# Optimization experiments

Hardware: AMD Instinct MI355X
Metric: run time of the kernel (lower is better)

## Reference

```python
import jax, jax.numpy as jnp
import numpy as np


def setup_inputs() -> dict:
    key = jax.random.key(0)
    k1, k2, k3, k4 = jax.random.split(key, 4)
    B, T, F_in, F_out, N, E, K = 16, 64, 64, 64, 128, 2, 4
    x = jax.random.normal(k1, (B, T, F_in, N), dtype=jnp.float32)
    # graph shift operator per (batch, time, edge-feature); scaled to keep powers bounded
    S = jax.random.normal(k2, (B, T, E, N, N), dtype=jnp.float32) / np.sqrt(N)
    H = jax.random.normal(k3, (F_out, E, K, F_in), dtype=jnp.float32) * 0.02
    bias = jax.random.normal(k4, (F_out, 1), dtype=jnp.float32) * 0.02
    return {"x": x, "S": S, "H": H, "bias": bias}


def reference(x, S, H, bias):
    # x: [B,T,F_in,N], S: [B,T,E,N,N], H: [F_out,E,K,F_in], bias: [F_out,1]
    B, T, F_in, N = x.shape
    E = S.shape[2]
    F_out, _, K, _ = H.shape
    # replicate features across edge-feature dim: [B,T,E,F_in,N]
    cur = jnp.broadcast_to(x[:, :, None], (B, T, E, F_in, N))
    taps = [cur]
    zero_row = jnp.zeros((B, 1, E, F_in, N), dtype=x.dtype)
    for _ in range(1, K):
        # time-shift: tap k at time t depends on tap k-1 at time t-1
        cur = jnp.concatenate([zero_row, cur[:, :-1]], axis=1)
        # diffuse over graph: [..,F_in,N] @ [..,N,N]
        cur = jnp.matmul(cur, S)
        taps.append(cur)
    z = jnp.stack(taps, axis=2)  # [B,T,K,E,F_in,N]
    # [B,T,N, E*K*F_in], matching permute(0,1,5,3,2,4) in the source
    z = z.transpose(0, 1, 5, 3, 2, 4).reshape(B, T, N, E * K * F_in)
    Hm = H.reshape(F_out, E * K * F_in)
    y = jnp.einsum('btnf,of->bton', z, Hm)  # [B,T,F_out,N]
    return y + bias  # bias [F_out,1] broadcasts over N
```

## Files before the change

kernel.cpp:

```cpp
#include <hip/hip_runtime.h>


namespace {
constexpr int B = 16, T = 64, F = 64, N = 128, E = 2, K = 4;
constexpr int SSW = 136;
constexpr int SXW = 68;
constexpr int SZW = 136;
constexpr int TC = 8;
}

typedef short v8s __attribute__((ext_vector_type(8)));
typedef float v4f __attribute__((ext_vector_type(4)));

__device__ inline ushort f2bf(float f) {
  union { float f; uint u; } v; v.f = f;
  uint u = v.u;
  return (ushort)((u + 0x7fffu + ((u >> 16) & 1u)) >> 16);
}

__device__ inline uint pk2(float a, float b) {
  return (uint)f2bf(a) | ((uint)f2bf(b) << 16);
}

__global__ __launch_bounds__(256, 2) void gf_fused(
    const float* __restrict__ x, const float* __restrict__ S,
    const float* __restrict__ H, const float* __restrict__ bias,
    float* __restrict__ y) {
  __shared__ ushort sS[128 * SSW];
  __shared__ ushort sX[128 * SXW];
  __shared__ ushort sSt[6][16 * SZW];
  const int g = blockIdx.x;
  const int xcd = g & 7, loc = g >> 3;
  const int os = loc & 3, unitL = loc >> 2;
  const int unit = xcd * 16 + unitL;
  const int b = unit >> 3, chunk = unit & 7;
  const int t0 = chunk * TC;
  const int ob = os * 16;
  const int tid = threadIdx.x, w = tid >> 6, lane = tid & 63;
  const int l15 = lane & 15, q = lane >> 4;

  for (int i = tid; i < 6 * 16 * SZW; i += 256) ((ushort*)sSt)[i] = 0;

  v4f Yac[2];
  Yac[0][0] = 0.f; Yac[0][1] = 0.f; Yac[0][2] = 0.f; Yac[0][3] = 0.f;
  Yac[1] = Yac[0];

  const int tstart = (t0 == 0) ? 0 : t0 - 3;
  for (int t = tstart; t < t0 + TC; ++t) {
    const bool skipS = (t0 != 0) && (t == t0 - 3);
    const bool emit = (t >= t0);

    {
      const float* xg = x + (size_t)(b * T + t) * (F * N);
      float4 r0[4], r1[4];
      #pragma unroll
      for (int it = 0; it < 4; ++it) {
        const int idx = tid + it * 256;
        const int m = idx >> 4, g2 = idx & 15;
        r0[it] = *(const float4*)(xg + m * N + g2 * 8);
        r1[it] = *(const float4*)(xg + m * N + g2 * 8 + 4);
      }
      #pragma unroll
      for (int it = 0; it < 4; ++it) {
        const int idx = tid + it * 256;
        const int m = idx >> 4, g2 = idx & 15;
        uint4 wv;
        wv.x = pk2(r0[it].x, r0[it].y); wv.y = pk2(r0[it].z, r0[it].w);
        wv.z = pk2(r1[it].x, r1[it].y); wv.w = pk2(r1[it].z, r1[it].w);
        *(uint4*)&sS[m * SSW + ((g2 ^ (m >> 3)) * 8)] = wv;
      }
      __syncthreads();
      const int bb = tid & 7, a2 = (tid >> 3) & 15, hh = tid >> 7;
      v8s rows[8];
      #pragma unroll
      for (int j = 0; j < 8; ++j)
        rows[j] = *(const v8s*)&sS[(8 * bb + j) * SSW + ((a2 ^ bb) * 8)];
      #pragma unroll
      for (int i = 0; i < 4; ++i) {
        const int e2 = 4 * hh + i;
        const int n = 8 * a2 + e2;
        uint4 wv;
        wv.x = (uint)(ushort)rows[0][e2] | ((uint)(ushort)rows[1][e2] << 16);
        wv.y = (uint)(ushort)rows[2][e2] | ((uint)(ushort)rows[3][e2] << 16);
        wv.z = (uint)(ushort)rows[4][e2] | ((uint)(ushort)rows[5][e2] << 16);
        wv.w = (uint)(ushort)rows[6][e2] | ((uint)(ushort)rows[7][e2] << 16);
        *(uint4*)&sX[n * SXW + 8 * bb] = wv;
      }
      __syncthreads();
    }

    for (int e = 0; e < E; ++e) {
      if (!skipS) {
        const float* Sg = S + (size_t)((b * T + t) * E + e) * (N * N);
        #pragma unroll
        for (int half = 0; half < 2; ++half) {
          float4 r0[4], r1[4];
          #pragma unroll
          for (int it = 0; it < 4; ++it) {
            const int idx = tid + (half * 4 + it) * 256;
            const int m = idx >> 4, g2 = idx & 15;
            r0[it] = *(const float4*)(Sg + m * N + g2 * 8);
            r1[it] = *(const float4*)(Sg + m * N + g2 * 8 + 4);
          }
          #pragma unroll
          for (int it = 0; it < 4; ++it) {
            const int idx = tid + (half * 4 + it) * 256;
            const int m = idx >> 4, g2 = idx & 15;
            uint4 wv;
            wv.x = pk2(r0[it].x, r0[it].y); wv.y = pk2(r0[it].z, r0[it].w);
            wv.z = pk2(r1[it].x, r1[it].y); wv.w = pk2(r1[it].z, r1[it].w);
            *(uint4*)&sS[m * SSW + ((g2 ^ (m >> 3)) * 8)] = wv;
          }
        }
      }

      v4f Pn[2], Qn[2], U3n[2];
      #pragma unroll
      for (int mt = 0; mt < 2; ++mt) {
        Pn[mt][0] = 0.f; Pn[mt][1] = 0.f; Pn[mt][2] = 0.f; Pn[mt][3] = 0.f;
        Qn[mt] = Pn[mt]; U3n[mt] = Pn[mt];
      }
      {
        const float* hrow = H + ((size_t)(ob + l15) * E + e) * K * F;
        v8s xf[2][2];
        #pragma unroll
        for (int mt = 0; mt < 2; ++mt)
          #pragma unroll
          for (int fk = 0; fk < 2; ++fk)
            xf[mt][fk] = *(const v8s*)&sX[((2 * w + mt) * 16 + l15) * SXW +
                                          fk * 32 + q * 8];
        #pragma unroll
        for (int k = 0; k < 4; ++k) {
          if (k == 0 && !emit) continue;
          v8s hf[2];
          #pragma unroll
          for (int fk = 0; fk < 2; ++fk) {
            const int f0 = fk * 32 + q * 8;
            const float4 h0 = *(const float4*)(hrow + k * F + f0);
            const float4 h1 = *(const float4*)(hrow + k * F + f0 + 4);
            uint4 u;
            u.x = pk2(h0.x, h0.y); u.y = pk2(h0.z, h0.w);
            u.z = pk2(h1.x, h1.y); u.w = pk2(h1.z, h1.w);
            union { uint4 u; v8s s; } cv; cv.u = u;
            hf[fk] = cv.s;
          }
          v4f* tgt = (k == 0) ? Yac : (k == 1 ? Pn : (k == 2 ? Qn : U3n));
          #pragma unroll
          for (int fk = 0; fk < 2; ++fk)
            #pragma unroll
            for (int mt = 0; mt < 2; ++mt)
              tgt[mt] = __builtin_amdgcn_mfma_f32_16x16x32_bf16(
                  xf[mt][fk], hf[fk], tgt[mt], 0, 0, 0);
        }
      }

      if (!skipS) {
        __syncthreads();
        const int a2 = tid & 15, bg = tid >> 4;
        v8s rows[8];
        #pragma unroll
        for (int j = 0; j < 8; ++j)
          rows[j] = *(const v8s*)&sS[(8 * a2 + j) * SSW + ((bg ^ a2) * 8)];
        __syncthreads();
        #pragma unroll
        for (int i = 0; i < 8; ++i) {
          uint4 wv;
          wv.x = (uint)(ushort)rows[0][i] | ((uint)(ushort)rows[1][i] << 16);
          wv.y = (uint)(ushort)rows[2][i] | ((uint)(ushort)rows[3][i] << 16);
          wv.z = (uint)(ushort)rows[4][i] | ((uint)(ushort)rows[5][i] << 16);
          wv.w = (uint)(ushort)rows[6][i] | ((uint)(ushort)rows[7][i] << 16);
          *(uint4*)&sS[(8 * bg + i) * SSW + ((a2 ^ bg) * 8)] = wv;
        }
        __syncthreads();
        #pragma unroll
        for (int c = 0; c < 4; ++c) {
          const int p = ((4 * c + q) + 2 * l15) & 15;
          const int sbase = l15 * SZW + p * 8;
          const v8s bzP = *(const v8s*)&sSt[e * 3 + 0][sbase];
          const v8s bzQ = *(const v8s*)&sSt[e * 3 + 1][sbase];
          const v8s bzU = *(const v8s*)&sSt[e * 3 + 2][sbase];
          #pragma unroll
          for (int mt = 0; mt < 2; ++mt) {
            const int n = (2 * w + mt) * 16 + l15;
            const v8s af = *(const v8s*)&sS[n * SSW +
                                            ((((c << 2) | q) ^ (n >> 3)) * 8)];
            if (emit)
              Yac[mt] = __builtin_amdgcn_mfma_f32_16x16x32_bf16(
                  af, bzP, Yac[mt], 0, 0, 0);
            Pn[mt] = __builtin_amdgcn_mfma_f32_16x16x32_bf16(
                af, bzQ, Pn[mt], 0, 0, 0);
            Qn[mt] = __builtin_amdgcn_mfma_f32_16x16x32_bf16(
                af, bzU, Qn[mt], 0, 0, 0);
          }
        }
      }

      __syncthreads();
      #pragma unroll
      for (int mt = 0; mt < 2; ++mt) {
        const int cc = (2 * w + mt) * 2 + (q >> 1), h = q & 1;
        const int p = (cc + 2 * l15) & 15;
        const int base = l15 * SZW + p * 8 + h * 4;
        uint2 wv;
        wv.x = pk2(Pn[mt][0], Pn[mt][1]); wv.y = pk2(Pn[mt][2], Pn[mt][3]);
        *(uint2*)&sSt[e * 3 + 0][base] = wv;
        wv.x = pk2(Qn[mt][0], Qn[mt][1]); wv.y = pk2(Qn[mt][2], Qn[mt][3]);
        *(uint2*)&sSt[e * 3 + 1][base] = wv;
        wv.x = pk2(U3n[mt][0], U3n[mt][1]); wv.y = pk2(U3n[mt][2], U3n[mt][3]);
        *(uint2*)&sSt[e * 3 + 2][base] = wv;
      }

      if (e == 1 && emit) {
        float* yg = y + (size_t)(b * T + t) * (F * N);
        const float bv = bias[ob + l15];
        #pragma unroll
        for (int mt = 0; mt < 2; ++mt) {
          float4 v;
          v.x = Yac[mt][0] + bv; v.y = Yac[mt][1] + bv;
          v.z = Yac[mt][2] + bv; v.w = Yac[mt][3] + bv;
          *(float4*)(yg + (ob + l15) * N + (2 * w + mt) * 16 + q * 4) = v;
          Yac[mt][0] = 0.f; Yac[mt][1] = 0.f;
          Yac[mt][2] = 0.f; Yac[mt][3] = 0.f;
        }
      }
    }
  }
}

extern "C" void kernel_launch(void* const* d_in, const int* in_sizes, int n_in,
                              void* d_out, int out_size, void* d_ws, size_t ws_size,
                              hipStream_t stream) {
  const float* x    = (const float*)d_in[0];
  const float* S    = (const float*)d_in[1];
  const float* H    = (const float*)d_in[2];
  const float* bias = (const float*)d_in[3];
  float* y = (float*)d_out;
  (void)d_ws; (void)ws_size;

  gf_fused<<<512, 256, 0, stream>>>(x, S, H, bias, y);
}
```

Before: 335.1 us.

## Pre-transpose x and H to bf16 in prep kernel and prefetch S into registers

```diff
diff --git a/kernel.cpp b/kernel.cpp
--- a/kernel.cpp
+++ b/kernel.cpp
@@ -4,7 +4,6 @@
 namespace {
 constexpr int B = 16, T = 64, F = 64, N = 128, E = 2, K = 4;
 constexpr int SSW = 136;
-constexpr int SXW = 68;
 constexpr int SZW = 136;
 constexpr int TC = 8;
 }
@@ -22,12 +21,70 @@
   return (uint)f2bf(a) | ((uint)f2bf(b) << 16);
 }
 
+__device__ inline void tr64x128(const float* __restrict__ src,
+                                ushort* __restrict__ dst, int dstride,
+                                ushort* sh, int tid) {
+  float4 r0[4], r1[4];
+  #pragma unroll
+  for (int it = 0; it < 4; ++it) {
+    const int idx = tid + it * 256;
+    const int m = idx >> 4, g = idx & 15;
+    r0[it] = *(const float4*)(src + m * N + g * 8);
+    r1[it] = *(const float4*)(src + m * N + g * 8 + 4);
+  }
+  #pragma unroll
+  for (int it = 0; it < 4; ++it) {
+    const int idx = tid + it * 256;
+    const int m = idx >> 4, g = idx & 15;
+    uint4 wv;
+    wv.x = pk2(r0[it].x, r0[it].y); wv.y = pk2(r0[it].z, r0[it].w);
+    wv.z = pk2(r1[it].x, r1[it].y); wv.w = pk2(r1[it].z, r1[it].w);
+    *(uint4*)&sh[m * SSW + ((g ^ (m >> 3)) * 8)] = wv;
+  }
+  __syncthreads();
+  const int bb = tid & 7, a = (tid >> 3) & 15, hh = tid >> 7;
+  v8s rows[8];
+  #pragma unroll
+  for (int j = 0; j < 8; ++j)
+    rows[j] = *(const v8s*)&sh[(8 * bb + j) * SSW + ((a ^ bb) * 8)];
+  #pragma unroll
+  for (int i = 0; i < 4; ++i) {
+    const int e = 4 * hh + i;
+    const int n = 8 * a + e;
+    uint4 wv;
+    wv.x = (uint)(ushort)rows[0][e] | ((uint)(ushort)rows[1][e] << 16);
+    wv.y = (uint)(ushort)rows[2][e] | ((uint)(ushort)rows[3][e] << 16);
+    wv.z = (uint)(ushort)rows[4][e] | ((uint)(ushort)rows[5][e] << 16);
+    wv.w = (uint)(ushort)rows[6][e] | ((uint)(ushort)rows[7][e] << 16);
+    *(uint4*)(dst + n * dstride + 8 * bb) = wv;
+  }
+}
+
+__global__ __launch_bounds__(256) void gf_prep(
+    const float* __restrict__ x, const float* __restrict__ H,
+    ushort* __restrict__ xT, ushort* __restrict__ Hb) {
+  __shared__ ushort sh[64 * SSW];
+  const int bid = blockIdx.x;
+  const int tid = threadIdx.x;
+  if (bid < B * T) {
+    tr64x128(x + (size_t)bid * F * N, xT + (size_t)bid * N * F, F, sh, tid);
+  } else {
+    const int hb = bid - B * T;
+    const int d = (hb * 256 + tid) * 4;
+    const int f = d & 63, o = (d >> 6) & 63, k = (d >> 12) & 3, e = (d >> 14) & 1;
+    const float4 v = *(const float4*)(H + (((size_t)o * E + e) * K + k) * F + f);
+    uint2 wv;
+    wv.x = pk2(v.x, v.y);
+    wv.y = pk2(v.z, v.w);
+    *(uint2*)(Hb + d) = wv;
+  }
+}
+
 __global__ __launch_bounds__(256, 2) void gf_fused(
-    const float* __restrict__ x, const float* __restrict__ S,
-    const float* __restrict__ H, const float* __restrict__ bias,
+    const float* __restrict__ S, const ushort* __restrict__ xT,
+    const ushort* __restrict__ Hb, const float* __restrict__ bias,
     float* __restrict__ y) {
   __shared__ ushort sS[128 * SSW];
-  __shared__ ushort sX[128 * SXW];
   __shared__ ushort sSt[6][16 * SZW];
   const int g = blockIdx.x;
   const int xcd = g & 7, loc = g >> 3;
@@ -46,70 +103,45 @@
   Yac[1] = Yac[0];
 
   const int tstart = (t0 == 0) ? 0 : t0 - 3;
+  const int tS0 = (t0 == 0) ? 0 : t0 - 2;
+
+  float4 pf0[8], pf1[8];
+  {
+    const float* Sg = S + (size_t)((b * T + tS0) * E + 0) * (N * N);
+    #pragma unroll
+    for (int j = 0; j < 8; ++j) {
+      const int idx = tid + j * 256;
+      const int m = idx >> 4, g2 = idx & 15;
+      pf0[j] = *(const float4*)(Sg + m * N + g2 * 8);
+      pf1[j] = *(const float4*)(Sg + m * N + g2 * 8 + 4);
+    }
+  }
+  __syncthreads();
+
   for (int t = tstart; t < t0 + TC; ++t) {
-    const bool skipS = (t0 != 0) && (t == t0 - 3);
+    const bool staged = (t >= tS0);
     const bool emit = (t >= t0);
-
-    {
-      const float* xg = x + (size_t)(b * T + t) * (F * N);
-      float4 r0[4], r1[4];
-      #pragma unroll
-      for (int it = 0; it < 4; ++it) {
-        const int idx = tid + it * 256;
-        const int m = idx >> 4, g2 = idx & 15;
-        r0[it] = *(const float4*)(xg + m * N + g2 * 8);
-        r1[it] = *(const float4*)(xg + m * N + g2 * 8 + 4);
-      }
-      #pragma unroll
-      for (int it = 0; it < 4; ++it) {
-        const int idx = tid + it * 256;
-        const int m = idx >> 4, g2 = idx & 15;
-        uint4 wv;
-        wv.x = pk2(r0[it].x, r0[it].y); wv.y = pk2(r0[it].z, r0[it].w);
-        wv.z = pk2(r1[it].x, r1[it].y); wv.w = pk2(r1[it].z, r1[it].w);
-        *(uint4*)&sS[m * SSW + ((g2 ^ (m >> 3)) * 8)] = wv;
-      }
-      __syncthreads();
-      const int bb = tid & 7, a2 = (tid >> 3) & 15, hh = tid >> 7;
-      v8s rows[8];
-      #pragma unroll
-      for (int j = 0; j < 8; ++j)
-        rows[j] = *(const v8s*)&sS[(8 * bb + j) * SSW + ((a2 ^ bb) * 8)];
-      #pragma unroll
-      for (int i = 0; i < 4; ++i) {
-        const int e2 = 4 * hh + i;
-        const int n = 8 * a2 + e2;
-        uint4 wv;
-        wv.x = (uint)(ushort)rows[0][e2] | ((uint)(ushort)rows[1][e2] << 16);
-        wv.y = (uint)(ushort)rows[2][e2] | ((uint)(ushort)rows[3][e2] << 16);
-        wv.z = (uint)(ushort)rows[4][e2] | ((uint)(ushort)rows[5][e2] << 16);
-        wv.w = (uint)(ushort)rows[6][e2] | ((uint)(ushort)rows[7][e2] << 16);
-        *(uint4*)&sX[n * SXW + 8 * bb] = wv;
-      }
-      __syncthreads();
-    }
-
     for (int e = 0; e < E; ++e) {
-      if (!skipS) {
-        const float* Sg = S + (size_t)((b * T + t) * E + e) * (N * N);
-        #pragma unroll
-        for (int half = 0; half < 2; ++half) {
-          float4 r0[4], r1[4];
-          #pragma unroll
-          for (int it = 0; it < 4; ++it) {
-            const int idx = tid + (half * 4 + it) * 256;
+      if (staged) {
+        #pragma unroll
+        for (int j = 0; j < 8; ++j) {
+          const int idx = tid + j * 256;
+          const int m = idx >> 4, g2 = idx & 15;
+          uint4 wv;
+          wv.x = pk2(pf0[j].x, pf0[j].y); wv.y = pk2(pf0[j].z, pf0[j].w);
+          wv.z = pk2(pf1[j].x, pf1[j].y); wv.w = pk2(pf1[j].z, pf1[j].w);
+          *(uint4*)&sS[m * SSW + ((g2 ^ (m >> 3)) * 8)] = wv;
+        }
+        const int nt = (e == 0) ? t : t + 1;
+        const int ne = (e == 0) ? 1 : 0;
+        if (nt < t0 + TC) {
+          const float* Sg = S + (size_t)((b * T + nt) * E + ne) * (N * N);
+          #pragma unroll
+          for (int j = 0; j < 8; ++j) {
+            const int idx = tid + j * 256;
             const int m = idx >> 4, g2 = idx & 15;
-            r0[it] = *(const float4*)(Sg + m * N + g2 * 8);
-            r1[it] = *(const float4*)(Sg + m * N + g2 * 8 + 4);
-          }
-          #pragma unroll
-          for (int it = 0; it < 4; ++it) {
-            const int idx = tid + (half * 4 + it) * 256;
-            const int m = idx >> 4, g2 = idx & 15;
-            uint4 wv;
-            wv.x = pk2(r0[it].x, r0[it].y); wv.y = pk2(r0[it].z, r0[it].w);
-            wv.z = pk2(r1[it].x, r1[it].y); wv.w = pk2(r1[it].z, r1[it].w);
-            *(uint4*)&sS[m * SSW + ((g2 ^ (m >> 3)) * 8)] = wv;
+            pf0[j] = *(const float4*)(Sg + m * N + g2 * 8);
+            pf1[j] = *(const float4*)(Sg + m * N + g2 * 8 + 4);
           }
         }
       }
@@ -121,29 +153,21 @@
         Qn[mt] = Pn[mt]; U3n[mt] = Pn[mt];
       }
       {
-        const float* hrow = H + ((size_t)(ob + l15) * E + e) * K * F;
+        const ushort* xrow = xT + (size_t)(b * T + t) * (N * F);
         v8s xf[2][2];
         #pragma unroll
         for (int mt = 0; mt < 2; ++mt)
           #pragma unroll
           for (int fk = 0; fk < 2; ++fk)
-            xf[mt][fk] = *(const v8s*)&sX[((2 * w + mt) * 16 + l15) * SXW +
-                                          fk * 32 + q * 8];
+            xf[mt][fk] = *(const v8s*)(xrow + ((2 * w + mt) * 16 + l15) * F +
+                                       fk * 32 + q * 8);
         #pragma unroll
         for (int k = 0; k < 4; ++k) {
           if (k == 0 && !emit) continue;
+          const ushort* hrow = Hb + ((size_t)((e * K + k) * 64) + ob + l15) * 64;
           v8s hf[2];
-          #pragma unroll
-          for (int fk = 0; fk < 2; ++fk) {
-            const int f0 = fk * 32 + q * 8;
-            const float4 h0 = *(const float4*)(hrow + k * F + f0);
-            const float4 h1 = *(const float4*)(hrow + k * F + f0 + 4);
-            uint4 u;
-            u.x = pk2(h0.x, h0.y); u.y = pk2(h0.z, h0.w);
-            u.z = pk2(h1.x, h1.y); u.w = pk2(h1.z, h1.w);
-            union { uint4 u; v8s s; } cv; cv.u = u;
-            hf[fk] = cv.s;
-          }
+          hf[0] = *(const v8s*)(hrow + q * 8);
+          hf[1] = *(const v8s*)(hrow + 32 + q * 8);
           v4f* tgt = (k == 0) ? Yac : (k == 1 ? Pn : (k == 2 ? Qn : U3n));
           #pragma unroll
           for (int fk = 0; fk < 2; ++fk)
@@ -154,7 +178,7 @@
         }
       }
 
-      if (!skipS) {
+      if (staged) {
         __syncthreads();
         const int a2 = tid & 15, bg = tid >> 4;
         v8s rows[8];
@@ -172,6 +196,7 @@
           *(uint4*)&sS[(8 * bg + i) * SSW + ((a2 ^ bg) * 8)] = wv;
         }
         __syncthreads();
+        __builtin_amdgcn_s_setprio(1);
         #pragma unroll
         for (int c = 0; c < 4; ++c) {
           const int p = ((4 * c + q) + 2 * l15) & 15;
@@ -193,6 +218,7 @@
                 af, bzU, Qn[mt], 0, 0, 0);
           }
         }
+        __builtin_amdgcn_s_setprio(0);
       }
 
       __syncthreads();
@@ -235,7 +261,11 @@
   const float* H    = (const float*)d_in[2];
   const float* bias = (const float*)d_in[3];
   float* y = (float*)d_out;
-  (void)d_ws; (void)ws_size;
-
-  gf_fused<<<512, 256, 0, stream>>>(x, S, H, bias, y);
-}
+
+  const size_t XTn = (size_t)B * T * N * F;
+  ushort* xT = (ushort*)d_ws;
+  ushort* Hb = xT + XTn;
+
+  gf_prep <<<B * T + 32, 256, 0, stream>>>(x, H, xT, Hb);
+  gf_fused<<<512,        256, 0, stream>>>(S, xT, Hb, bias, y);
+}
```

Measured after the change: 294.5 us. 1.14x faster.
